# Kernel optimization log

Hardware: AMD Instinct MI355X
Metric: run time of the kernel (lower is better)

## Reference

```python
import jax, jax.numpy as jnp
import numpy as np

B = 2048
PARAM_SHAPES = {
    'l1c0': (1, 8, 3, 3), 'l1c1': (3, 4, 8, 2), 'l1c2': (2, 4, 8, 2), 'l1c3': (2, 4, 8, 2), 'l1c4': (2, 4, 8, 1), 'b1': (8, 4, 4, 4, 4),
    'l2c0': (1, 4, 8, 2), 'l2c1': (2, 2, 4, 2), 'l2c2': (2, 2, 4, 2), 'l2c3': (2, 2, 4, 2), 'l2c4': (2, 2, 4, 1), 'b2': (4, 2, 2, 2, 2),
    'l3c0': (1, 2, 4, 2), 'l3c1': (2, 2, 2, 2), 'l3c2': (2, 2, 2, 2), 'l3c3': (2, 2, 2, 2), 'l3c4': (2, 2, 2, 1), 'b3': (2, 2, 2, 2, 2),
    'W': (2, 32), 'bl': (2,),
}

def setup_inputs():
    key = jax.random.key(0)
    ks = jax.random.split(key, len(PARAM_SHAPES) + 1)
    inp = {'x': jax.random.normal(ks[0], (B, 3, 8, 8, 8, 8), dtype=jnp.float32)}
    for k, (name, shp) in zip(ks[1:], PARAM_SHAPES.items()):
        scale = 0.5 if name[0] == 'l' and name != 'bl' else 0.1
        inp[name] = jax.random.normal(k, shp, dtype=jnp.float32) * scale
    return inp

def tt_linear(x, cores, bias):
    # y[b, m1..md] = sum_{n1..nd} W[m1..md, n1..nd] x[b, n1..nd] + bias[m1..md]
    # W is the TT-matrix with cores G_k of shape (r_{k-1}, m_k, n_k, r_k).
    b = x.shape[0]
    z = x.reshape(b, 1, -1)  # (B, rank, flat=[n_k..n_d, m_1..m_{k-1}])
    for G in cores:
        r0, m, n, r1 = G.shape
        z = jnp.einsum('brns,rmnq->bqsm', z.reshape(b, r0, n, -1), G).reshape(b, r1, -1)
    return z.reshape((b,) + bias.shape) + bias

def reference(x, l1c0, l1c1, l1c2, l1c3, l1c4, b1, l2c0, l2c1, l2c2, l2c3, l2c4, b2, l3c0, l3c1, l3c2, l3c3, l3c4, b3, W, bl):
    h = jax.nn.relu(tt_linear(x, [l1c0, l1c1, l1c2, l1c3, l1c4], b1))
    h = jax.nn.relu(tt_linear(h, [l2c0, l2c1, l2c2, l2c3, l2c4], b2))
    h = jax.nn.relu(tt_linear(h, [l3c0, l3c1, l3c2, l3c3, l3c4], b3))
    logits = h.reshape(-1, 32) @ W.T + bl  # (B, 2)
    return jax.nn.log_softmax(logits, axis=1)
```

## Files before the change

### kernel.cpp

```cpp
#include <hip/hip_runtime.h>
#include <math.h>

#define LC4   0
#define LC3   64
#define LC2   192
#define LC1   320
#define LC0   512
#define LU4   584
#define LU3   600
#define LU2   632
#define LU1   664
#define LU0   696
#define LB2   760
#define LB3   824
#define LWH   856
#define LBL   920
#define LW3   924
#define T2O   2972
#define T3O   9308
#define H1O   9308
#define T4O   2972
#define L2AO  2972
#define L2BO  5532
#define L2CO  6684
#define L2DO  7228
#define H2O   7500
#define H3O   7564
#define LDS_FLOATS 12476

__global__ void tt_setup_w3(const float* __restrict__ v0, const float* __restrict__ v1,
                            const float* __restrict__ v2, const float* __restrict__ v3,
                            const float* __restrict__ v4, float* __restrict__ w3) {
    int i = blockIdx.x * 256 + threadIdx.x;
    if (i >= 2048) return;
    int mi = i >> 6, nj = i & 63;
    int m1 = (mi >> 4) & 1, m2 = (mi >> 3) & 1, m3 = (mi >> 2) & 1, m4 = (mi >> 1) & 1, m5 = mi & 1;
    int n1 = (nj >> 4) & 3, n2 = (nj >> 3) & 1, n3 = (nj >> 2) & 1, n4 = (nj >> 1) & 1, n5 = nj & 1;
    float s = 0.f;
#pragma unroll
    for (int q1 = 0; q1 < 2; ++q1) {
        float a1 = v0[(m1 * 4 + n1) * 2 + q1];
#pragma unroll
        for (int q2 = 0; q2 < 2; ++q2) {
            float a2 = a1 * v1[((q1 * 2 + m2) * 2 + n2) * 2 + q2];
#pragma unroll
            for (int q3 = 0; q3 < 2; ++q3) {
                float a3 = a2 * v2[((q2 * 2 + m3) * 2 + n3) * 2 + q3];
#pragma unroll
                for (int q4 = 0; q4 < 2; ++q4)
                    s = fmaf(a3 * v3[((q3 * 2 + m4) * 2 + n4) * 2 + q4],
                             v4[(q4 * 2 + m5) * 2 + n5], s);
            }
        }
    }
    w3[i] = s;
}

__global__ __launch_bounds__(192)
void tt_main(const float* __restrict__ x,
             const float* __restrict__ g0, const float* __restrict__ g1,
             const float* __restrict__ g2, const float* __restrict__ g3,
             const float* __restrict__ g4, const float* __restrict__ b1g,
             const float* __restrict__ u0, const float* __restrict__ u1,
             const float* __restrict__ u2, const float* __restrict__ u3,
             const float* __restrict__ u4, const float* __restrict__ b2g,
             const float* __restrict__ b3g,
             const float* __restrict__ Wmg, const float* __restrict__ blg,
             const float* __restrict__ w3g,
             float* __restrict__ out)
{
    __shared__ float smem[LDS_FLOATS];
    const int t = threadIdx.x;
    const int b = blockIdx.x;

    if (t < 64)  smem[LC4 + t] = g4[t];
    if (t < 128) smem[LC3 + t] = g3[t];
    if (t < 128) smem[LC2 + t] = g2[t];
    smem[LC1 + t] = g1[t];
    if (t < 72)  smem[LC0 + t] = g0[t];
    if (t < 16)  smem[LU4 + t] = u4[t];
    if (t < 32)  smem[LU3 + t] = u3[t];
    if (t < 32)  smem[LU2 + t] = u2[t];
    if (t < 32)  smem[LU1 + t] = u1[t];
    if (t < 64)  smem[LU0 + t] = u0[t];
    if (t < 64)  smem[LB2 + t] = b2g[t];
    if (t < 32)  smem[LB3 + t] = b3g[t];
    if (t < 64)  smem[LWH + t] = Wmg[t];
    if (t < 2)   smem[LBL + t] = blg[t];
#pragma unroll
    for (int i = t; i < 2048; i += 192) smem[LW3 + i] = w3g[i];

    float accT2[32];
#pragma unroll
    for (int i = 0; i < 32; ++i) accT2[i] = 0.f;
    const float* xp = x + (size_t)b * 12288 + t * 64;

    __syncthreads();

#pragma unroll
    for (int h = 0; h < 2; ++h) {
        float xv[32];
        const float4* xp4 = (const float4*)(xp + h * 32);
#pragma unroll
        for (int i = 0; i < 8; ++i) {
            float4 v = xp4[i];
            xv[i * 4 + 0] = v.x; xv[i * 4 + 1] = v.y; xv[i * 4 + 2] = v.z; xv[i * 4 + 3] = v.w;
        }
        float t1[32];
#pragma unroll
        for (int m5 = 0; m5 < 4; ++m5)
#pragma unroll
        for (int q4 = 0; q4 < 2; ++q4) {
            float w[8];
#pragma unroll
            for (int n5 = 0; n5 < 8; ++n5) w[n5] = smem[LC4 + (q4 * 4 + m5) * 8 + n5];
#pragma unroll
            for (int n4l = 0; n4l < 4; ++n4l) {
                float s = 0.f;
#pragma unroll
                for (int n5 = 0; n5 < 8; ++n5) s = fmaf(xv[n4l * 8 + n5], w[n5], s);
                t1[(n4l * 4 + m5) * 2 + q4] = s;
            }
        }
#pragma unroll
        for (int q3 = 0; q3 < 2; ++q3)
#pragma unroll
        for (int m4 = 0; m4 < 4; ++m4) {
            float cs[8];
#pragma unroll
            for (int k = 0; k < 8; ++k) cs[k] = smem[LC3 + ((q3 * 4 + m4) * 8 + h * 4) * 2 + k];
#pragma unroll
            for (int m5 = 0; m5 < 4; ++m5) {
                float s = accT2[(m4 * 4 + m5) * 2 + q3];
#pragma unroll
                for (int n4l = 0; n4l < 4; ++n4l)
#pragma unroll
                for (int q4 = 0; q4 < 2; ++q4)
                    s = fmaf(t1[(n4l * 4 + m5) * 2 + q4], cs[n4l * 2 + q4], s);
                accT2[(m4 * 4 + m5) * 2 + q3] = s;
            }
        }
    }
#pragma unroll
    for (int j = 0; j < 32; ++j) smem[T2O + t * 33 + j] = accT2[j];
    __syncthreads();

    {
        const int q2 = t & 1, m3 = (t >> 1) & 3, nn = t >> 3;
        float o3[16];
#pragma unroll
        for (int i = 0; i < 16; ++i) o3[i] = 0.f;
#pragma unroll
        for (int n3 = 0; n3 < 8; ++n3) {
            const int rb = T2O + (nn * 8 + n3) * 33;
            const float w0 = smem[LC2 + ((q2 * 4 + m3) * 8 + n3) * 2 + 0];
            const float w1 = smem[LC2 + ((q2 * 4 + m3) * 8 + n3) * 2 + 1];
#pragma unroll
            for (int m45 = 0; m45 < 16; ++m45) {
                const float z0 = smem[rb + m45 * 2 + 0];
                const float z1 = smem[rb + m45 * 2 + 1];
                o3[m45] = fmaf(z0, w0, fmaf(z1, w1, o3[m45]));
            }
        }
        const int wb = T3O + (nn * 4 + m3) * 33;
#pragma unroll
        for (int m45 = 0; m45 < 16; ++m45) smem[wb + m45 * 2 + q2] = o3[m45];
    }
    __syncthreads();

    {
        const int n1 = t >> 6, m2 = (t >> 4) & 3, m3 = (t >> 2) & 3, m4 = t & 3;
        float o4[12];
#pragma unroll
        for (int i = 0; i < 12; ++i) o4[i] = 0.f;
#pragma unroll
        for (int n2 = 0; n2 < 8; ++n2) {
            float tv[8];
            const int rb = T3O + ((n1 * 8 + n2) * 4 + m3) * 33 + m4 * 8;
#pragma unroll
            for (int k = 0; k < 8; ++k) tv[k] = smem[rb + k];
#pragma unroll
            for (int q2 = 0; q2 < 2; ++q2)
#pragma unroll
            for (int q1 = 0; q1 < 3; ++q1) {
                const float w = smem[LC1 + ((q1 * 4 + m2) * 8 + n2) * 2 + q2];
#pragma unroll
                for (int m5 = 0; m5 < 4; ++m5)
                    o4[m5 * 3 + q1] = fmaf(tv[m5 * 2 + q2], w, o4[m5 * 3 + q1]);
            }
        }
        const int bj = m2 * 64 + m3 * 16 + m4 * 4;
#pragma unroll
        for (int m5 = 0; m5 < 4; ++m5)
#pragma unroll
        for (int q1 = 0; q1 < 3; ++q1)
            smem[T4O + (bj + m5) * 9 + n1 * 3 + q1] = o4[m5 * 3 + q1];
    }
    __syncthreads();

#pragma unroll
    for (int r = 0; r < 2; ++r) {
        const int j = t + r * 192;
        if (j < 256) {
            float o5[8];
#pragma unroll
            for (int i = 0; i < 8; ++i) o5[i] = 0.f;
#pragma unroll
            for (int n1 = 0; n1 < 3; ++n1)
#pragma unroll
            for (int q1 = 0; q1 < 3; ++q1) {
                const float tv = smem[T4O + j * 9 + n1 * 3 + q1];
#pragma unroll
                for (int m1 = 0; m1 < 8; ++m1)
                    o5[m1] = fmaf(tv, smem[LC0 + (m1 * 3 + n1) * 3 + q1], o5[m1]);
            }
#pragma unroll
            for (int m1 = 0; m1 < 8; ++m1)
                smem[H1O + m1 * 256 + j] = fmaxf(o5[m1] + b1g[m1 * 256 + j], 0.f);
        }
    }
    __syncthreads();

#pragma unroll
    for (int r = 0; r < 3; ++r) {
        const int P = t + r * 192;
        if (P < 512) {
            float hv[4];
#pragma unroll
            for (int n5 = 0; n5 < 4; ++n5) hv[n5] = smem[H1O + P * 4 + n5];
#pragma unroll
            for (int m5 = 0; m5 < 2; ++m5)
#pragma unroll
            for (int q4 = 0; q4 < 2; ++q4) {
                float s = 0.f;
#pragma unroll
                for (int n5 = 0; n5 < 4; ++n5)
                    s = fmaf(hv[n5], smem[LU4 + (q4 * 2 + m5) * 4 + n5], s);
                smem[L2AO + P * 5 + m5 * 2 + q4] = s;
            }
        }
    }
    __syncthreads();

    if (t < 128) {
        float o[8];
#pragma unroll
        for (int i = 0; i < 8; ++i) o[i] = 0.f;
#pragma unroll
        for (int n4 = 0; n4 < 4; ++n4)
#pragma unroll
        for (int q4 = 0; q4 < 2; ++q4) {
            const float a0 = smem[L2AO + (t * 4 + n4) * 5 + 0 * 2 + q4];
            const float a1 = smem[L2AO + (t * 4 + n4) * 5 + 1 * 2 + q4];
#pragma unroll
            for (int q3 = 0; q3 < 2; ++q3)
#pragma unroll
            for (int m4 = 0; m4 < 2; ++m4) {
                const float w = smem[LU3 + ((q3 * 2 + m4) * 4 + n4) * 2 + q4];
                o[(m4 * 2 + 0) * 2 + q3] = fmaf(a0, w, o[(m4 * 2 + 0) * 2 + q3]);
                o[(m4 * 2 + 1) * 2 + q3] = fmaf(a1, w, o[(m4 * 2 + 1) * 2 + q3]);
            }
        }
#pragma unroll
        for (int k = 0; k < 8; ++k) smem[L2BO + t * 9 + k] = o[k];
    }
    __syncthreads();

    if (t < 32) {
        float o[16];
#pragma unroll
        for (int i = 0; i < 16; ++i) o[i] = 0.f;
#pragma unroll
        for (int n3 = 0; n3 < 4; ++n3)
#pragma unroll
        for (int q3 = 0; q3 < 2; ++q3) {
            float zb[4];
#pragma unroll
            for (int m45 = 0; m45 < 4; ++m45)
                zb[m45] = smem[L2BO + (t * 4 + n3) * 9 + m45 * 2 + q3];
#pragma unroll
            for (int m3 = 0; m3 < 2; ++m3)
#pragma unroll
            for (int q2 = 0; q2 < 2; ++q2) {
                const float w = smem[LU2 + ((q2 * 2 + m3) * 4 + n3) * 2 + q3];
#pragma unroll
                for (int m45 = 0; m45 < 4; ++m45)
                    o[(m3 * 4 + m45) * 2 + q2] = fmaf(zb[m45], w, o[(m3 * 4 + m45) * 2 + q2]);
            }
        }
#pragma unroll
        for (int k = 0; k < 16; ++k) smem[L2CO + t * 17 + k] = o[k];
    }
    __syncthreads();

    if (t < 32) {
        const int n1 = t >> 2, m2 = (t >> 1) & 1, m3 = t & 1;
        float o[8];
#pragma unroll
        for (int i = 0; i < 8; ++i) o[i] = 0.f;
#pragma unroll
        for (int n2 = 0; n2 < 4; ++n2)
#pragma unroll
        for (int q2 = 0; q2 < 2; ++q2) {
            float cb[4];
#pragma unroll
            for (int m45 = 0; m45 < 4; ++m45)
                cb[m45] = smem[L2CO + (n1 * 4 + n2) * 17 + (m3 * 4 + m45) * 2 + q2];
#pragma unroll
            for (int q1 = 0; q1 < 2; ++q1) {
                const float w = smem[LU1 + ((q1 * 2 + m2) * 4 + n2) * 2 + q2];
#pragma unroll
                for (int m45 = 0; m45 < 4; ++m45)
                    o[m45 * 2 + q1] = fmaf(cb[m45], w, o[m45 * 2 + q1]);
            }
        }
#pragma unroll
        for (int m45 = 0; m45 < 4; ++m45)
#pragma unroll
        for (int q1 = 0; q1 < 2; ++q1)
            smem[L2DO + (m2 * 8 + m3 * 4 + m45) * 17 + n1 * 2 + q1] = o[m45 * 2 + q1];
    }
    __syncthreads();

    if (t < 16) {
        float o[4];
#pragma unroll
        for (int i = 0; i < 4; ++i) o[i] = 0.f;
#pragma unroll
        for (int n1 = 0; n1 < 8; ++n1)
#pragma unroll
        for (int q1 = 0; q1 < 2; ++q1) {
            const float dv = smem[L2DO + t * 17 + n1 * 2 + q1];
#pragma unroll
            for (int m1 = 0; m1 < 4; ++m1)
                o[m1] = fmaf(dv, smem[LU0 + (m1 * 8 + n1) * 2 + q1], o[m1]);
        }
#pragma unroll
        for (int m1 = 0; m1 < 4; ++m1)
            smem[H2O + m1 * 16 + t] = fmaxf(o[m1] + smem[LB2 + m1 * 16 + t], 0.f);
    }
    __syncthreads();

    if (t < 32) {
        float s = smem[LB3 + t];
#pragma unroll
        for (int k = 0; k < 64; ++k) {
            const int kk = (k + t) & 63;
            s = fmaf(smem[LW3 + t * 64 + kk], smem[H2O + kk], s);
        }
        smem[H3O + t] = fmaxf(s, 0.f);
    }
    __syncthreads();

    if (t < 64) {
        const int c = t >> 5, k = t & 31;
        float pr = smem[H3O + k] * smem[LWH + c * 32 + k];
#pragma unroll
        for (int d = 16; d >= 1; d >>= 1) pr += __shfl_xor(pr, d);
        const float l0 = __shfl(pr, 0) + smem[LBL + 0];
        const float l1 = __shfl(pr, 32) + smem[LBL + 1];
        if (t == 0) {
            const float mm = fmaxf(l0, l1);
            const float lse = mm + logf(expf(l0 - mm) + expf(l1 - mm));
            out[(size_t)b * 2 + 0] = l0 - lse;
            out[(size_t)b * 2 + 1] = l1 - lse;
        }
    }
}

extern "C" void kernel_launch(void* const* d_in, const int* in_sizes, int n_in,
                              void* d_out, int out_size, void* d_ws, size_t ws_size,
                              hipStream_t stream) {
    const float* x    = (const float*)d_in[0];
    const float* l1c0 = (const float*)d_in[1];
    const float* l1c1 = (const float*)d_in[2];
    const float* l1c2 = (const float*)d_in[3];
    const float* l1c3 = (const float*)d_in[4];
    const float* l1c4 = (const float*)d_in[5];
    const float* b1   = (const float*)d_in[6];
    const float* l2c0 = (const float*)d_in[7];
    const float* l2c1 = (const float*)d_in[8];
    const float* l2c2 = (const float*)d_in[9];
    const float* l2c3 = (const float*)d_in[10];
    const float* l2c4 = (const float*)d_in[11];
    const float* b2   = (const float*)d_in[12];
    const float* l3c0 = (const float*)d_in[13];
    const float* l3c1 = (const float*)d_in[14];
    const float* l3c2 = (const float*)d_in[15];
    const float* l3c3 = (const float*)d_in[16];
    const float* l3c4 = (const float*)d_in[17];
    const float* b3   = (const float*)d_in[18];
    const float* Wm   = (const float*)d_in[19];
    const float* bl   = (const float*)d_in[20];
    float* W3 = (float*)d_ws;

    tt_setup_w3<<<8, 256, 0, stream>>>(l3c0, l3c1, l3c2, l3c3, l3c4, W3);
    tt_main<<<2048, 192, 0, stream>>>(x, l1c0, l1c1, l1c2, l1c3, l1c4, b1,
                                      l2c0, l2c1, l2c2, l2c3, l2c4, b2, b3,
                                      Wm, bl, W3, (float*)d_out);
}
```

Measured before the change: 220.9 us.

## Restructure TT layer-1 into single-wave blocks with streamed x slices and small LDS

Each batch block now runs on a single 64-thread wavefront instead of 192 threads. Layer 1 is processed as six streamed slices of x, and the next slice is prefetched into registers while the current one is computed. Partial contractions are kept in registers and combined via shuffles, which shrinks LDS use from about 49KB to about 18KB. Most small weights are now read directly from global/constant memory instead of being staged in LDS, and W3 is read straight from global. The goal is higher occupancy and fewer LDS round trips. The costs are more sequential work per wave, more barriers inside the slice loop, and heavy register pressure from the xv/xn/t1/regT4 arrays.

Result: faster. 209.1 us (-5.3%).

```diff
diff --git a/kernel.cpp b/kernel.cpp
--- a/kernel.cpp
+++ b/kernel.cpp
@@ -1,32 +1,19 @@
 #include <hip/hip_runtime.h>
 #include <math.h>
 
-#define LC4   0
-#define LC3   64
-#define LC2   192
-#define LC1   320
-#define LC0   512
-#define LU4   584
-#define LU3   600
-#define LU2   632
-#define LU1   664
-#define LU0   696
-#define LB2   760
-#define LB3   824
-#define LWH   856
-#define LBL   920
-#define LW3   924
-#define T2O   2972
-#define T3O   9308
-#define H1O   9308
-#define T4O   2972
-#define L2AO  2972
-#define L2BO  5532
-#define L2CO  6684
-#define L2DO  7228
-#define H2O   7500
-#define H3O   7564
-#define LDS_FLOATS 12476
+#define WC3  0
+#define WC2  128
+#define WU1  256
+#define T2S  288
+#define T3S  1440
+#define H1O  288
+#define AO   2528
+#define BO   288
+#define CO   1440
+#define DO   1984
+#define H2O  2256
+#define H3O  2320
+#define LDS_FLOATS 4576
 
 __global__ void tt_setup_w3(const float* __restrict__ v0, const float* __restrict__ v1,
                             const float* __restrict__ v2, const float* __restrict__ v3,
@@ -56,7 +43,7 @@
     w3[i] = s;
 }
 
-__global__ __launch_bounds__(192)
+__global__ __launch_bounds__(64, 2)
 void tt_main(const float* __restrict__ x,
              const float* __restrict__ g0, const float* __restrict__ g1,
              const float* __restrict__ g2, const float* __restrict__ g3,
@@ -72,197 +59,217 @@
     __shared__ float smem[LDS_FLOATS];
     const int t = threadIdx.x;
     const int b = blockIdx.x;
-
-    if (t < 64)  smem[LC4 + t] = g4[t];
-    if (t < 128) smem[LC3 + t] = g3[t];
-    if (t < 128) smem[LC2 + t] = g2[t];
-    smem[LC1 + t] = g1[t];
-    if (t < 72)  smem[LC0 + t] = g0[t];
-    if (t < 16)  smem[LU4 + t] = u4[t];
-    if (t < 32)  smem[LU3 + t] = u3[t];
-    if (t < 32)  smem[LU2 + t] = u2[t];
-    if (t < 32)  smem[LU1 + t] = u1[t];
-    if (t < 64)  smem[LU0 + t] = u0[t];
-    if (t < 64)  smem[LB2 + t] = b2g[t];
-    if (t < 32)  smem[LB3 + t] = b3g[t];
-    if (t < 64)  smem[LWH + t] = Wmg[t];
-    if (t < 2)   smem[LBL + t] = blg[t];
-#pragma unroll
-    for (int i = t; i < 2048; i += 192) smem[LW3 + i] = w3g[i];
-
-    float accT2[32];
-#pragma unroll
-    for (int i = 0; i < 32; ++i) accT2[i] = 0.f;
-    const float* xp = x + (size_t)b * 12288 + t * 64;
-
-    __syncthreads();
-
-#pragma unroll
-    for (int h = 0; h < 2; ++h) {
-        float xv[32];
-        const float4* xp4 = (const float4*)(xp + h * 32);
+    const float* xb = x + (size_t)b * 12288;
+
+    float xv[32];
+    {
+        const float4* xq = (const float4*)xb + t * 8;
 #pragma unroll
         for (int i = 0; i < 8; ++i) {
-            float4 v = xp4[i];
-            xv[i * 4 + 0] = v.x; xv[i * 4 + 1] = v.y; xv[i * 4 + 2] = v.z; xv[i * 4 + 3] = v.w;
-        }
-        float t1[32];
-#pragma unroll
-        for (int m5 = 0; m5 < 4; ++m5)
+            const float4 v = xq[i];
+            xv[i*4+0] = v.x; xv[i*4+1] = v.y; xv[i*4+2] = v.z; xv[i*4+3] = v.w;
+        }
+    }
+
+    smem[WC3 + t] = g3[t];  smem[WC3 + 64 + t] = g3[64 + t];
+    smem[WC2 + t] = g2[t];  smem[WC2 + 64 + t] = g2[64 + t];
+    if (t < 32) smem[WU1 + t] = u1[t];
+    __syncthreads();
+
+    const int h = t & 1;
+    const int p = t >> 1;
+
+    float regT4[36];
+#pragma unroll
+    for (int i = 0; i < 36; ++i) regT4[i] = 0.f;
+
+#pragma unroll
+    for (int n1 = 0; n1 < 3; ++n1) {
+#pragma unroll
+        for (int n2h = 0; n2h < 2; ++n2h) {
+            const int s = n1 * 2 + n2h;
+            float xn[32];
+            if (s < 5) {
+                const float4* xq = (const float4*)xb + (s + 1) * 512 + t * 8;
+#pragma unroll
+                for (int i = 0; i < 8; ++i) {
+                    const float4 v = xq[i];
+                    xn[i*4+0] = v.x; xn[i*4+1] = v.y; xn[i*4+2] = v.z; xn[i*4+3] = v.w;
+                }
+            }
+
+            float t1[32];
+#pragma unroll
+            for (int m5 = 0; m5 < 4; ++m5)
+#pragma unroll
+            for (int q4 = 0; q4 < 2; ++q4) {
+                const float* w = g4 + (q4 * 4 + m5) * 8;
+#pragma unroll
+                for (int n4l = 0; n4l < 4; ++n4l) {
+                    float sa = xv[n4l*8+0] * w[0];
+#pragma unroll
+                    for (int n5 = 1; n5 < 8; ++n5) sa = fmaf(xv[n4l*8+n5], w[n5], sa);
+                    t1[n4l*8 + m5*2 + q4] = sa;
+                }
+            }
+
+            float acc[16];
+#pragma unroll
+            for (int i = 0; i < 16; ++i) acc[i] = 0.f;
+#pragma unroll
+            for (int pass = 0; pass < 2; ++pass) {
+                const int hh = (pass == 0) ? h : (1 - h);
+                if (pass == 1) {
+#pragma unroll
+                    for (int i = 0; i < 32; ++i) t1[i] = __shfl_xor(t1[i], 1);
+                }
+#pragma unroll
+                for (int m4 = 0; m4 < 4; ++m4) {
+                    const int cbase = WC3 + ((h * 4 + m4) * 8 + hh * 4) * 2;
+                    const float4 c0 = *(const float4*)&smem[cbase];
+                    const float4 c1 = *(const float4*)&smem[cbase + 4];
+                    const float cs[8] = {c0.x, c0.y, c0.z, c0.w, c1.x, c1.y, c1.z, c1.w};
+#pragma unroll
+                    for (int m5 = 0; m5 < 4; ++m5) {
+                        float sa = acc[m4*4+m5];
+#pragma unroll
+                        for (int n4l = 0; n4l < 4; ++n4l)
+#pragma unroll
+                        for (int q4 = 0; q4 < 2; ++q4)
+                            sa = fmaf(t1[n4l*8 + m5*2 + q4], cs[n4l*2 + q4], sa);
+                        acc[m4*4+m5] = sa;
+                    }
+                }
+            }
+
+            __syncthreads();
+#pragma unroll
+            for (int m45 = 0; m45 < 16; ++m45)
+                smem[T2S + p * 36 + m45 * 2 + h] = acc[m45];
+            __syncthreads();
+
+            {
+                const int n3h = t & 1;
+                const int q2  = (t >> 1) & 1;
+                const int m3  = (t >> 2) & 3;
+                const int n2l = t >> 4;
+                float o3[16];
+#pragma unroll
+                for (int i = 0; i < 16; ++i) o3[i] = 0.f;
+#pragma unroll
+                for (int n3l = 0; n3l < 4; ++n3l) {
+                    const int rb = T2S + (n2l * 8 + n3h * 4 + n3l) * 36;
+                    float rv[32];
+#pragma unroll
+                    for (int g = 0; g < 8; ++g) {
+                        const float4 v = *(const float4*)&smem[rb + g * 4];
+                        rv[g*4+0] = v.x; rv[g*4+1] = v.y; rv[g*4+2] = v.z; rv[g*4+3] = v.w;
+                    }
+                    const int wb = WC2 + ((q2 * 4 + m3) * 8 + n3h * 4 + n3l) * 2;
+                    const float w0 = smem[wb], w1 = smem[wb + 1];
+#pragma unroll
+                    for (int m45 = 0; m45 < 16; ++m45)
+                        o3[m45] = fmaf(rv[m45*2], w0, fmaf(rv[m45*2+1], w1, o3[m45]));
+                }
+#pragma unroll
+                for (int k = 0; k < 16; ++k) o3[k] += __shfl_xor(o3[k], 1);
+                const int row = n2h * 16 + n2l * 4 + m3;
+#pragma unroll
+                for (int k = 0; k < 8; ++k) {
+                    const float v = n3h ? o3[8 + k] : o3[k];
+                    smem[T3S + row * 34 + (n3h * 8 + k) * 2 + q2] = v;
+                }
+            }
+            if (s < 5) {
+#pragma unroll
+                for (int i = 0; i < 32; ++i) xv[i] = xn[i];
+            }
+        }
+        __syncthreads();
+
+        {
+            const int m3 = t >> 4, m4 = (t >> 2) & 3, m5 = t & 3;
+            float2 zz[8];
+#pragma unroll
+            for (int n2 = 0; n2 < 8; ++n2)
+                zz[n2] = *(const float2*)&smem[T3S + (n2 * 4 + m3) * 34 + (m4 * 4 + m5) * 2];
+#pragma unroll
+            for (int jj = 0; jj < 4; ++jj)
+#pragma unroll
+            for (int q1 = 0; q1 < 3; ++q1) {
+                float sa = regT4[jj * 9 + n1 * 3 + q1];
+#pragma unroll
+                for (int n2g = 0; n2g < 4; ++n2g) {
+                    const float4 w = *(const float4*)(g1 + ((q1 * 4 + jj) * 8 + n2g * 2) * 2);
+                    sa = fmaf(zz[n2g*2].x,   w.x, sa);
+                    sa = fmaf(zz[n2g*2].y,   w.y, sa);
+                    sa = fmaf(zz[n2g*2+1].x, w.z, sa);
+                    sa = fmaf(zz[n2g*2+1].y, w.w, sa);
+                }
+                regT4[jj * 9 + n1 * 3 + q1] = sa;
+            }
+        }
+    }
+    __syncthreads();
+
+#pragma unroll
+    for (int jj = 0; jj < 4; ++jj) {
+        float bia[8];
+#pragma unroll
+        for (int m1 = 0; m1 < 8; ++m1) bia[m1] = b1g[m1 * 256 + jj * 64 + t];
+#pragma unroll
+        for (int m1 = 0; m1 < 8; ++m1) {
+            float sa = bia[m1];
+#pragma unroll
+            for (int n1 = 0; n1 < 3; ++n1)
+#pragma unroll
+            for (int q1 = 0; q1 < 3; ++q1)
+                sa = fmaf(regT4[jj * 9 + n1 * 3 + q1], g0[(m1 * 3 + n1) * 3 + q1], sa);
+            smem[H1O + m1 * 256 + jj * 64 + t] = fmaxf(sa, 0.f);
+        }
+    }
+    __syncthreads();
+
+#pragma unroll
+    for (int pp = 0; pp < 8; ++pp) {
+        const int P = pp * 64 + t;
+        const float4 hv = *(const float4*)&smem[H1O + P * 4];
+        float4 av;
+        av.x = hv.x*u4[0]  + hv.y*u4[1]  + hv.z*u4[2]  + hv.w*u4[3];
+        av.y = hv.x*u4[8]  + hv.y*u4[9]  + hv.z*u4[10] + hv.w*u4[11];
+        av.z = hv.x*u4[4]  + hv.y*u4[5]  + hv.z*u4[6]  + hv.w*u4[7];
+        av.w = hv.x*u4[12] + hv.y*u4[13] + hv.z*u4[14] + hv.w*u4[15];
+        *(float4*)&smem[AO + P * 4] = av;
+    }
+    __syncthreads();
+
+#pragma unroll
+    for (int pp = 0; pp < 2; ++pp) {
+        const int p3 = pp * 64 + t;
+        float4 aa[4];
+#pragma unroll
+        for (int n4 = 0; n4 < 4; ++n4)
+            aa[n4] = *(const float4*)&smem[AO + (p3 * 4 + n4) * 4];
+        float o[8];
+#pragma unroll
+        for (int i = 0; i < 8; ++i) o[i] = 0.f;
+#pragma unroll
+        for (int n4 = 0; n4 < 4; ++n4)
 #pragma unroll
         for (int q4 = 0; q4 < 2; ++q4) {
-            float w[8];
-#pragma unroll
-            for (int n5 = 0; n5 < 8; ++n5) w[n5] = smem[LC4 + (q4 * 4 + m5) * 8 + n5];
-#pragma unroll
-            for (int n4l = 0; n4l < 4; ++n4l) {
-                float s = 0.f;
-#pragma unroll
-                for (int n5 = 0; n5 < 8; ++n5) s = fmaf(xv[n4l * 8 + n5], w[n5], s);
-                t1[(n4l * 4 + m5) * 2 + q4] = s;
-            }
-        }
-#pragma unroll
-        for (int q3 = 0; q3 < 2; ++q3)
-#pragma unroll
-        for (int m4 = 0; m4 < 4; ++m4) {
-            float cs[8];
-#pragma unroll
-            for (int k = 0; k < 8; ++k) cs[k] = smem[LC3 + ((q3 * 4 + m4) * 8 + h * 4) * 2 + k];
-#pragma unroll
-            for (int m5 = 0; m5 < 4; ++m5) {
-                float s = accT2[(m4 * 4 + m5) * 2 + q3];
-#pragma unroll
-                for (int n4l = 0; n4l < 4; ++n4l)
-#pragma unroll
-                for (int q4 = 0; q4 < 2; ++q4)
-                    s = fmaf(t1[(n4l * 4 + m5) * 2 + q4], cs[n4l * 2 + q4], s);
-                accT2[(m4 * 4 + m5) * 2 + q3] = s;
-            }
-        }
-    }
-#pragma unroll
-    for (int j = 0; j < 32; ++j) smem[T2O + t * 33 + j] = accT2[j];
-    __syncthreads();
-
-    {
-        const int q2 = t & 1, m3 = (t >> 1) & 3, nn = t >> 3;
-        float o3[16];
-#pragma unroll
-        for (int i = 0; i < 16; ++i) o3[i] = 0.f;
-#pragma unroll
-        for (int n3 = 0; n3 < 8; ++n3) {
-            const int rb = T2O + (nn * 8 + n3) * 33;
-            const float w0 = smem[LC2 + ((q2 * 4 + m3) * 8 + n3) * 2 + 0];
-            const float w1 = smem[LC2 + ((q2 * 4 + m3) * 8 + n3) * 2 + 1];
-#pragma unroll
-            for (int m45 = 0; m45 < 16; ++m45) {
-                const float z0 = smem[rb + m45 * 2 + 0];
-                const float z1 = smem[rb + m45 * 2 + 1];
-                o3[m45] = fmaf(z0, w0, fmaf(z1, w1, o3[m45]));
-            }
-        }
-        const int wb = T3O + (nn * 4 + m3) * 33;
-#pragma unroll
-        for (int m45 = 0; m45 < 16; ++m45) smem[wb + m45 * 2 + q2] = o3[m45];
-    }
-    __syncthreads();
-
-    {
-        const int n1 = t >> 6, m2 = (t >> 4) & 3, m3 = (t >> 2) & 3, m4 = t & 3;
-        float o4[12];
-#pragma unroll
-        for (int i = 0; i < 12; ++i) o4[i] = 0.f;
-#pragma unroll
-        for (int n2 = 0; n2 < 8; ++n2) {
-            float tv[8];
-            const int rb = T3O + ((n1 * 8 + n2) * 4 + m3) * 33 + m4 * 8;
-#pragma unroll
-            for (int k = 0; k < 8; ++k) tv[k] = smem[rb + k];
-#pragma unroll
-            for (int q2 = 0; q2 < 2; ++q2)
-#pragma unroll
-            for (int q1 = 0; q1 < 3; ++q1) {
-                const float w = smem[LC1 + ((q1 * 4 + m2) * 8 + n2) * 2 + q2];
-#pragma unroll
-                for (int m5 = 0; m5 < 4; ++m5)
-                    o4[m5 * 3 + q1] = fmaf(tv[m5 * 2 + q2], w, o4[m5 * 3 + q1]);
-            }
-        }
-        const int bj = m2 * 64 + m3 * 16 + m4 * 4;
-#pragma unroll
-        for (int m5 = 0; m5 < 4; ++m5)
-#pragma unroll
-        for (int q1 = 0; q1 < 3; ++q1)
-            smem[T4O + (bj + m5) * 9 + n1 * 3 + q1] = o4[m5 * 3 + q1];
-    }
-    __syncthreads();
-
-#pragma unroll
-    for (int r = 0; r < 2; ++r) {
-        const int j = t + r * 192;
-        if (j < 256) {
-            float o5[8];
-#pragma unroll
-            for (int i = 0; i < 8; ++i) o5[i] = 0.f;
-#pragma unroll
-            for (int n1 = 0; n1 < 3; ++n1)
-#pragma unroll
-            for (int q1 = 0; q1 < 3; ++q1) {
-                const float tv = smem[T4O + j * 9 + n1 * 3 + q1];
-#pragma unroll
-                for (int m1 = 0; m1 < 8; ++m1)
-                    o5[m1] = fmaf(tv, smem[LC0 + (m1 * 3 + n1) * 3 + q1], o5[m1]);
-            }
-#pragma unroll
-            for (int m1 = 0; m1 < 8; ++m1)
-                smem[H1O + m1 * 256 + j] = fmaxf(o5[m1] + b1g[m1 * 256 + j], 0.f);
-        }
-    }
-    __syncthreads();
-
-#pragma unroll
-    for (int r = 0; r < 3; ++r) {
-        const int P = t + r * 192;
-        if (P < 512) {
-            float hv[4];
-#pragma unroll
-            for (int n5 = 0; n5 < 4; ++n5) hv[n5] = smem[H1O + P * 4 + n5];
-#pragma unroll
-            for (int m5 = 0; m5 < 2; ++m5)
-#pragma unroll
-            for (int q4 = 0; q4 < 2; ++q4) {
-                float s = 0.f;
-#pragma unroll
-                for (int n5 = 0; n5 < 4; ++n5)
-                    s = fmaf(hv[n5], smem[LU4 + (q4 * 2 + m5) * 4 + n5], s);
-                smem[L2AO + P * 5 + m5 * 2 + q4] = s;
-            }
-        }
-    }
-    __syncthreads();
-
-    if (t < 128) {
-        float o[8];
-#pragma unroll
-        for (int i = 0; i < 8; ++i) o[i] = 0.f;
-#pragma unroll
-        for (int n4 = 0; n4 < 4; ++n4)
-#pragma unroll
-        for (int q4 = 0; q4 < 2; ++q4) {
-            const float a0 = smem[L2AO + (t * 4 + n4) * 5 + 0 * 2 + q4];
-            const float a1 = smem[L2AO + (t * 4 + n4) * 5 + 1 * 2 + q4];
+            const float a0 = q4 ? aa[n4].y : aa[n4].x;
+            const float a1 = q4 ? aa[n4].w : aa[n4].z;
 #pragma unroll
             for (int q3 = 0; q3 < 2; ++q3)
 #pragma unroll
             for (int m4 = 0; m4 < 2; ++m4) {
-                const float w = smem[LU3 + ((q3 * 2 + m4) * 4 + n4) * 2 + q4];
+                const float w = u3[((q3 * 2 + m4) * 4 + n4) * 2 + q4];
                 o[(m4 * 2 + 0) * 2 + q3] = fmaf(a0, w, o[(m4 * 2 + 0) * 2 + q3]);
                 o[(m4 * 2 + 1) * 2 + q3] = fmaf(a1, w, o[(m4 * 2 + 1) * 2 + q3]);
             }
         }
 #pragma unroll
-        for (int k = 0; k < 8; ++k) smem[L2BO + t * 9 + k] = o[k];
+        for (int k = 0; k < 8; ++k) smem[BO + p3 * 9 + k] = o[k];
     }
     __syncthreads();
 
@@ -277,19 +284,19 @@
             float zb[4];
 #pragma unroll
             for (int m45 = 0; m45 < 4; ++m45)
-                zb[m45] = smem[L2BO + (t * 4 + n3) * 9 + m45 * 2 + q3];
+                zb[m45] = smem[BO + (t * 4 + n3) * 9 + m45 * 2 + q3];
 #pragma unroll
             for (int m3 = 0; m3 < 2; ++m3)
 #pragma unroll
             for (int q2 = 0; q2 < 2; ++q2) {
-                const float w = smem[LU2 + ((q2 * 2 + m3) * 4 + n3) * 2 + q3];
+                const float w = u2[((q2 * 2 + m3) * 4 + n3) * 2 + q3];
 #pragma unroll
                 for (int m45 = 0; m45 < 4; ++m45)
                     o[(m3 * 4 + m45) * 2 + q2] = fmaf(zb[m45], w, o[(m3 * 4 + m45) * 2 + q2]);
             }
         }
 #pragma unroll
-        for (int k = 0; k < 16; ++k) smem[L2CO + t * 17 + k] = o[k];
+        for (int k = 0; k < 16; ++k) smem[CO + t * 17 + k] = o[k];
     }
     __syncthreads();
 
@@ -305,10 +312,10 @@
             float cb[4];
 #pragma unroll
             for (int m45 = 0; m45 < 4; ++m45)
-                cb[m45] = smem[L2CO + (n1 * 4 + n2) * 17 + (m3 * 4 + m45) * 2 + q2];
+                cb[m45] = smem[CO + (n1 * 4 + n2) * 17 + (m3 * 4 + m45) * 2 + q2];
 #pragma unroll
             for (int q1 = 0; q1 < 2; ++q1) {
-                const float w = smem[LU1 + ((q1 * 2 + m2) * 4 + n2) * 2 + q2];
+                const float w = smem[WU1 + ((q1 * 2 + m2) * 4 + n2) * 2 + q2];
 #pragma unroll
                 for (int m45 = 0; m45 < 4; ++m45)
                     o[m45 * 2 + q1] = fmaf(cb[m45], w, o[m45 * 2 + q1]);
@@ -318,7 +325,7 @@
         for (int m45 = 0; m45 < 4; ++m45)
 #pragma unroll
         for (int q1 = 0; q1 < 2; ++q1)
-            smem[L2DO + (m2 * 8 + m3 * 4 + m45) * 17 + n1 * 2 + q1] = o[m45 * 2 + q1];
+            smem[DO + (m2 * 8 + m3 * 4 + m45) * 17 + n1 * 2 + q1] = o[m45 * 2 + q1];
     }
     __syncthreads();
 
@@ -330,35 +337,39 @@
         for (int n1 = 0; n1 < 8; ++n1)
 #pragma unroll
         for (int q1 = 0; q1 < 2; ++q1) {
-            const float dv = smem[L2DO + t * 17 + n1 * 2 + q1];
+            const float dv = smem[DO + t * 17 + n1 * 2 + q1];
 #pragma unroll
             for (int m1 = 0; m1 < 4; ++m1)
-                o[m1] = fmaf(dv, smem[LU0 + (m1 * 8 + n1) * 2 + q1], o[m1]);
+                o[m1] = fmaf(dv, u0[(m1 * 8 + n1) * 2 + q1], o[m1]);
         }
 #pragma unroll
         for (int m1 = 0; m1 < 4; ++m1)
-            smem[H2O + m1 * 16 + t] = fmaxf(o[m1] + smem[LB2 + m1 * 16 + t], 0.f);
+            smem[H2O + m1 * 16 + t] = fmaxf(o[m1] + b2g[m1 * 16 + t], 0.f);
     }
     __syncthreads();
 
     if (t < 32) {
-        float s = smem[LB3 + t];
-#pragma unroll
-        for (int k = 0; k < 64; ++k) {
-            const int kk = (k + t) & 63;
-            s = fmaf(smem[LW3 + t * 64 + kk], smem[H2O + kk], s);
-        }
-        smem[H3O + t] = fmaxf(s, 0.f);
-    }
-    __syncthreads();
-
-    if (t < 64) {
-        const int c = t >> 5, k = t & 31;
-        float pr = smem[H3O + k] * smem[LWH + c * 32 + k];
+        const float4* wr = (const float4*)(w3g + t * 64);
+        float sa = b3g[t];
+#pragma unroll
+        for (int g = 0; g < 16; ++g) {
+            const float4 w4 = wr[g];
+            sa = fmaf(w4.x, smem[H2O + g*4 + 0],
+                 fmaf(w4.y, smem[H2O + g*4 + 1],
+                 fmaf(w4.z, smem[H2O + g*4 + 2],
+                 fmaf(w4.w, smem[H2O + g*4 + 3], sa))));
+        }
+        smem[H3O + t] = fmaxf(sa, 0.f);
+    }
+    __syncthreads();
+
+    {
+        const int k = t & 31;
+        float pr = smem[H3O + k] * Wmg[t];
 #pragma unroll
         for (int d = 16; d >= 1; d >>= 1) pr += __shfl_xor(pr, d);
-        const float l0 = __shfl(pr, 0) + smem[LBL + 0];
-        const float l1 = __shfl(pr, 32) + smem[LBL + 1];
+        const float l0 = __shfl(pr, 0) + blg[0];
+        const float l1 = __shfl(pr, 32) + blg[1];
         if (t == 0) {
             const float mm = fmaxf(l0, l1);
             const float lse = mm + logf(expf(l0 - mm) + expf(l1 - mm));
@@ -395,7 +406,7 @@
     float* W3 = (float*)d_ws;
 
     tt_setup_w3<<<8, 256, 0, stream>>>(l3c0, l3c1, l3c2, l3c3, l3c4, W3);
-    tt_main<<<2048, 192, 0, stream>>>(x, l1c0, l1c1, l1c2, l1c3, l1c4, b1,
-                                      l2c0, l2c1, l2c2, l2c3, l2c4, b2, b3,
-                                      Wm, bl, W3, (float*)d_out);
+    tt_main<<<2048, 64, 0, stream>>>(x, l1c0, l1c1, l1c2, l1c3, l1c4, b1,
+                                     l2c0, l2c1, l2c2, l2c3, l2c4, b2, b3,
+                                     Wm, bl, W3, (float*)d_out);
 }
```
